# Kernel optimization log

Hardware: AMD Instinct MI355X
Metric: run time of the kernel (lower is better)

## Reference

```python
import jax, jax.numpy as jnp
import numpy as np

B, H, W, N, P = 8, 640, 640, 12, 256
MIN_PATCH_AREA = 4.0
SQRT2 = 1.41421356237
DEG20 = 20.0 * np.pi / 180.0
TOL = 0.2  # center jitter tolerance


def setup_inputs() -> dict:
    key = jax.random.key(0)
    k_img, k_patch, k_y, k_h, k_x, k_w = jax.random.split(key, 6)
    images = jax.random.uniform(k_img, (B, H, W, 3), minval=-1.0, maxval=1.0, dtype=jnp.float32)
    patch = jax.random.uniform(k_patch, (P, P, 3), minval=-1.0, maxval=1.0, dtype=jnp.float32)
    ymin = jax.random.uniform(k_y, (B, N), minval=0.0, maxval=H - 220.0)
    bh = jax.random.uniform(k_h, (B, N), minval=40.0, maxval=200.0)
    xmin = jax.random.uniform(k_x, (B, N), minval=0.0, maxval=W - 220.0)
    bw = jax.random.uniform(k_w, (B, N), minval=40.0, maxval=200.0)
    boxes = jnp.stack([ymin, xmin, ymin + bh, xmin + bw], axis=-1).astype(jnp.float32)
    scale = jnp.float32(0.4)
    return {"images": images, "boxes": boxes, "patch": patch, "scale": scale}


def _bilinear(img, py, px):
    # img: [P,P,3]; py/px: [H,W] continuous source coords; edge-clamped bilinear
    Pd = img.shape[0]
    y0 = jnp.floor(py); x0 = jnp.floor(px)
    wy = (py - y0)[..., None]; wx = (px - x0)[..., None]
    y0i = jnp.clip(y0.astype(jnp.int32), 0, Pd - 1)
    x0i = jnp.clip(x0.astype(jnp.int32), 0, Pd - 1)
    y1i = jnp.clip(y0i + 1, 0, Pd - 1)
    x1i = jnp.clip(x0i + 1, 0, Pd - 1)
    v00 = img[y0i, x0i]; v01 = img[y0i, x1i]
    v10 = img[y1i, x0i]; v11 = img[y1i, x1i]
    return (1 - wy) * ((1 - wx) * v00 + wx * v01) + wy * ((1 - wx) * v10 + wx * v11)


def _apply_box(image, patch_m, box, key, scale, yy, xx):
    kc1, kc2, ka, kd, kn = jax.random.split(key, 5)
    ymin, xmin, ymax, xmax = box[0], box[1], box[2], box[3]
    h = ymax - ymin; w = xmax - xmin
    longer = jnp.maximum(h, w)
    patch_size = jnp.floor(longer * scale)          # create(): floor(longer*scale)
    diag = jnp.minimum(SQRT2 * patch_size, float(W))
    jy = (jax.random.uniform(kc1, ()) - 0.5) * TOL * h
    jx = (jax.random.uniform(kc2, ()) - 0.5) * TOL * w
    oy = ymin + h / 2.0 + jy
    ox = xmin + w / 2.0 + jx
    ymin_p = jnp.maximum(oy - diag / 2.0, 0.0)
    xmin_p = jnp.maximum(ox - diag / 2.0, 0.0)
    ymin_p = jnp.where(ymin_p + diag > H, H - diag, ymin_p)
    xmin_p = jnp.where(xmin_p + diag > W, W - diag, xmin_p)
    valid_box = patch_size * patch_size > MIN_PATCH_AREA  # min-area filter
    # int32 casts in tf == floor on nonnegative values
    y0f = jnp.floor(ymin_p); x0f = jnp.floor(xmin_p)
    phf = patch_size; diagf = jnp.floor(diag)
    top = jnp.floor((diagf - phf) / 2.0)            # pad offset
    angle = (jax.random.uniform(ka, ()) * 2.0 - 1.0) * DEG20
    delta = (jax.random.uniform(kd, ()) * 2.0 - 1.0) * 0.3  # random_brightness
    # inverse warp: image pixel -> padded-rotated patch coords
    u = yy - y0f; v = xx - x0f
    inside = (u >= 0) & (u < diagf) & (v >= 0) & (v < diagf)
    c = (diagf - 1.0) / 2.0
    ca = jnp.cos(angle); sa = jnp.sin(angle)
    sv = ca * (v - c) - sa * (u - c) + c
    su = sa * (v - c) + ca * (u - c) + c
    ry = su - top; rx = sv - top                     # coords in resized ph x pw patch
    src_ok = (ry >= 0) & (ry <= phf - 1) & (rx >= 0) & (rx <= phf - 1)
    safe_ph = jnp.maximum(phf, 1.0)
    py = (ry + 0.5) * (P / safe_ph) - 0.5            # half-pixel-center resize map
    px = (rx + 0.5) * (P / safe_ph) - 0.5
    vals = _bilinear(patch_m, py, px)                # [H,W,3]
    noise = jax.random.uniform(kn, vals.shape, minval=-0.01, maxval=0.01)
    vals = jnp.clip(vals + noise + delta, -1.0, 1.0)
    mask = (inside & src_ok & valid_box)[..., None]
    return jnp.where(mask, vals, image)              # tensor_scatter_nd_update + bg fill


def _patch_one_image(image, boxes, patch, scale, key):
    kw, kb, ks = jax.random.split(key, 3)
    wmul = 0.5 + 0.1 * jax.random.normal(kw, (1, 1, 3))
    badd = 0.01 * jax.random.normal(kb, (1, 1, 3))
    p = jnp.clip(wmul * patch + badd, -1.0, 1.0)     # random_print_adjust
    p = jnp.clip(p + (jnp.mean(image) - jnp.mean(p)), -1.0, 1.0)  # brightness match
    yy, xx = jnp.meshgrid(jnp.arange(H, dtype=jnp.float32),
                          jnp.arange(W, dtype=jnp.float32), indexing="ij")
    box_keys = jax.random.split(ks, boxes.shape[0])

    def body(img, bk):
        box, k = bk
        return _apply_box(img, p, box, k, scale, yy, xx), None

    img, _ = jax.lax.scan(body, image, (boxes, box_keys))
    return img


def reference(images, boxes, patch, scale):
    key = jax.random.key(42)
    img_keys = jax.random.split(key, images.shape[0])
    return jax.vmap(lambda im, bx, k: _patch_one_image(im, bx, patch, scale, k))(images, boxes, img_keys)
```

## Files before the change

kernel.cpp:

```cpp
#include <hip/hip_runtime.h>
#include <stdint.h>


#define IMG_ELEMS   1228800
#define NPIX        409600
#define PATCH_ELEMS 196608
#define WB_OFF 2048
#define BP_OFF 2112

#define TF_R(r) { x0 += x1; x1 = (x1 << r) | (x1 >> (32 - r)); x1 ^= x0; }

__device__ __forceinline__ void tf2x32(uint32_t k0, uint32_t k1,
                                       uint32_t c0, uint32_t c1,
                                       uint32_t& o0, uint32_t& o1) {
  uint32_t k2 = k0 ^ k1 ^ 0x1BD11BDAu;
  uint32_t x0 = c0 + k0, x1 = c1 + k1;
  TF_R(13) TF_R(15) TF_R(26) TF_R(6)
  x0 += k1; x1 += k2 + 1u;
  TF_R(17) TF_R(29) TF_R(16) TF_R(24)
  x0 += k2; x1 += k0 + 2u;
  TF_R(13) TF_R(15) TF_R(26) TF_R(6)
  x0 += k0; x1 += k1 + 3u;
  TF_R(17) TF_R(29) TF_R(16) TF_R(24)
  x0 += k1; x1 += k2 + 4u;
  TF_R(13) TF_R(15) TF_R(26) TF_R(6)
  x0 += k2; x1 += k0 + 5u;
  o0 = x0; o1 = x1;
}

__device__ __forceinline__ void split_key(uint32_t k0, uint32_t k1, uint32_t j,
                                          uint32_t& o0, uint32_t& o1) {
  tf2x32(k0, k1, 0u, j, o0, o1);
}

__device__ __forceinline__ uint32_t rbits32(uint32_t k0, uint32_t k1, uint32_t i) {
  uint32_t o0, o1;
  tf2x32(k0, k1, 0u, i, o0, o1);
  return o0 ^ o1;
}

__device__ __forceinline__ float u01(uint32_t bits) {
  return __uint_as_float((bits >> 9) | 0x3f800000u) - 1.0f;
}

__device__ __forceinline__ float erfinv_f(float x) {
  #pragma clang fp contract(off)
  float w = -log1pf(-(x * x));
  float p;
  if (w < 5.0f) {
    w = w - 2.5f;
    p = 2.81022636e-08f;
    p = 3.43273939e-07f + p * w;
    p = -3.5233877e-06f + p * w;
    p = -4.39150654e-06f + p * w;
    p = 0.00021858087f + p * w;
    p = -0.00125372503f + p * w;
    p = -0.00417768164f + p * w;
    p = 0.246640727f + p * w;
    p = 1.50140941f + p * w;
  } else {
    w = sqrtf(w) - 3.0f;
    p = -0.000200214257f;
    p = 0.000100950558f + p * w;
    p = 0.00134934322f + p * w;
    p = -0.00367342844f + p * w;
    p = 0.00573950773f + p * w;
    p = -0.0076224613f + p * w;
    p = 0.00943887047f + p * w;
    p = 1.00167406f + p * w;
    p = 2.83297682f + p * w;
  }
  return p * x;
}

__device__ __forceinline__ void wb_compute(int b, float* wm, float* bd) {
  #pragma clang fp contract(off)
  uint32_t ik0, ik1; split_key(0u, 42u, (uint32_t)b, ik0, ik1);
  uint32_t kw0, kw1; split_key(ik0, ik1, 0u, kw0, kw1);
  uint32_t kb0, kb1; split_key(ik0, ik1, 1u, kb0, kb1);
  const float lo  = __uint_as_float(0xBF7FFFFFu);
  const float SQ2 = (float)1.4142135623730951;
  for (int c = 0; c < 3; ++c) {
    float f  = u01(rbits32(kw0, kw1, (uint32_t)c));
    float u  = fmaxf(lo, __fadd_rn(__fmul_rn(f, 2.0f), lo));
    wm[c] = __fadd_rn(0.5f, __fmul_rn(0.1f, __fmul_rn(SQ2, erfinv_f(u))));
    float f2 = u01(rbits32(kb0, kb1, (uint32_t)c));
    float u2 = fmaxf(lo, __fadd_rn(__fmul_rn(f2, 2.0f), lo));
    bd[c] = __fmul_rn(0.01f, __fmul_rn(SQ2, erfinv_f(u2)));
  }
}

__global__ __launch_bounds__(256) void k_sums(const float4* __restrict__ img,
                                              const float4* __restrict__ patch,
                                              const float* __restrict__ boxes,
                                              const float* __restrict__ scale_p,
                                              float* __restrict__ wsf) {
  #pragma clang fp contract(off)
  int b = blockIdx.y;
  int bx = blockIdx.x;
  double* Pd = (double*)wsf;
  int tid = threadIdx.x;

  if (bx == 120) {
    if (b != 0) return;
    float scale = scale_p[0];
    if (tid < 8) {
      float wm[3], bd[3];
      wb_compute(tid, wm, bd);
      #pragma unroll
      for (int c = 0; c < 3; ++c) {
        wsf[WB_OFF + tid * 8 + c] = wm[c];
        wsf[WB_OFF + tid * 8 + 4 + c] = bd[c];
      }
    }
    if (tid >= 32 && tid < 128) {
      int t = tid - 32;
      int ib = t / 12, n = t % 12;
      uint32_t ik0, ik1; split_key(0u, 42u, (uint32_t)ib, ik0, ik1);
      uint32_t ks0, ks1; split_key(ik0, ik1, 2u, ks0, ks1);
      uint32_t bk0, bk1; split_key(ks0, ks1, (uint32_t)n, bk0, bk1);
      uint32_t kc10, kc11; split_key(bk0, bk1, 0u, kc10, kc11);
      uint32_t kc20, kc21; split_key(bk0, bk1, 1u, kc20, kc21);
      uint32_t ka0,  ka1;  split_key(bk0, bk1, 2u, ka0,  ka1);
      uint32_t kd0,  kd1;  split_key(bk0, bk1, 3u, kd0,  kd1);
      uint32_t kn0,  kn1;  split_key(bk0, bk1, 4u, kn0,  kn1);

      const float* bxp = boxes + (ib * 12 + n) * 4;
      float ymin = bxp[0], xmin = bxp[1], ymax = bxp[2], xmax = bxp[3];
      float h  = __fsub_rn(ymax, ymin);
      float ww = __fsub_rn(xmax, xmin);
      float longer = fmaxf(h, ww);
      float patch_size = floorf(__fmul_rn(longer, scale));
      float diag = fminf(__fmul_rn((float)1.41421356237, patch_size), 640.0f);
      float u1 = u01(rbits32(kc10, kc11, 0u));
      float u2 = u01(rbits32(kc20, kc21, 0u));
      float jy = __fmul_rn(__fmul_rn(__fsub_rn(u1, 0.5f), 0.2f), h);
      float jx = __fmul_rn(__fmul_rn(__fsub_rn(u2, 0.5f), 0.2f), ww);
      float oy = __fadd_rn(__fadd_rn(ymin, __fmul_rn(h, 0.5f)), jy);
      float ox = __fadd_rn(__fadd_rn(xmin, __fmul_rn(ww, 0.5f)), jx);
      float ymin_p = fmaxf(__fsub_rn(oy, __fmul_rn(diag, 0.5f)), 0.0f);
      float xmin_p = fmaxf(__fsub_rn(ox, __fmul_rn(diag, 0.5f)), 0.0f);
      ymin_p = (__fadd_rn(ymin_p, diag) > 640.0f) ? __fsub_rn(640.0f, diag) : ymin_p;
      xmin_p = (__fadd_rn(xmin_p, diag) > 640.0f) ? __fsub_rn(640.0f, diag) : xmin_p;
      float valid = (__fmul_rn(patch_size, patch_size) > 4.0f) ? 1.0f : 0.0f;
      float y0f = floorf(ymin_p), x0f = floorf(xmin_p);
      float phf = patch_size, diagf = floorf(diag);
      float top = floorf(__fmul_rn(__fsub_rn(diagf, phf), 0.5f));
      float ua = u01(rbits32(ka0, ka1, 0u));
      float angle = __fmul_rn(__fsub_rn(__fmul_rn(ua, 2.0f), 1.0f),
                              (float)0.3490658503988659);
      float ud = u01(rbits32(kd0, kd1, 0u));
      float delta = __fmul_rn(__fsub_rn(__fmul_rn(ud, 2.0f), 1.0f), 0.3f);
      float cc = __fmul_rn(__fsub_rn(diagf, 1.0f), 0.5f);
      float ca = (float)cos((double)angle);
      float sa = (float)sin((double)angle);
      float safe_ph = fmaxf(phf, 1.0f);
      float q = __fdiv_rn(256.0f, safe_ph);

      float* Pp = wsf + BP_OFF + (ib * 12 + n) * 16;
      Pp[0] = y0f;  Pp[1] = x0f;  Pp[2] = diagf; Pp[3] = phf;
      Pp[4] = top;  Pp[5] = cc;   Pp[6] = ca;    Pp[7] = sa;
      Pp[8] = delta; Pp[9] = valid;
      Pp[10] = __uint_as_float(kn0); Pp[11] = __uint_as_float(kn1);
      Pp[12] = q;
    }
    return;
  }

  double s = 0.0;
  int slot;
  if (bx < 120) {
    slot = b * 120 + bx;
    const float4* p = img + (size_t)b * (IMG_ELEMS / 4);
    const uint32_t stride = 120u * 256u;
    for (uint32_t i = bx * 256u + tid; i < (uint32_t)(IMG_ELEMS / 4); i += stride) {
      float4 v = p[i];
      s += (double)v.x + (double)v.y + (double)v.z + (double)v.w;
    }
  } else {
    slot = 960 + b * 8 + (bx - 121);
    __shared__ float pwb[8];
    if (tid == 0) {
      float wm[3], bd[3];
      wb_compute(b, wm, bd);
      #pragma unroll
      for (int c = 0; c < 3; ++c) { pwb[c] = wm[c]; pwb[4 + c] = bd[c]; }
    }
    __syncthreads();
    float wm[3] = {pwb[0], pwb[1], pwb[2]};
    float bd[3] = {pwb[4], pwb[5], pwb[6]};
    const uint32_t stride = 8u * 256u;
    for (uint32_t i = (bx - 121u) * 256u + tid; i < (uint32_t)(PATCH_ELEMS / 4);
         i += stride) {
      float4 v = patch[i];
      uint32_t c = (4u * i) % 3u;
      float f[4] = {v.x, v.y, v.z, v.w};
      #pragma unroll
      for (int j = 0; j < 4; ++j) {
        float val = __fadd_rn(__fmul_rn(wm[c], f[j]), bd[c]);
        val = fminf(fmaxf(val, -1.0f), 1.0f);
        s += (double)val;
        c = (c == 2u) ? 0u : (c + 1u);
      }
    }
  }
  for (int off = 32; off > 0; off >>= 1) s += __shfl_down(s, off, 64);
  __shared__ double sd[4];
  if ((tid & 63) == 0) sd[tid >> 6] = s;
  __syncthreads();
  if (tid == 0) Pd[slot] = sd[0] + sd[1] + sd[2] + sd[3];
}

__global__ __launch_bounds__(256) void k_main(const float4* __restrict__ img4,
                                              const float* __restrict__ wsf,
                                              const float* __restrict__ patch,
                                              float4* __restrict__ out4) {
  #pragma clang fp contract(off)
  __shared__ float bp[192];
  __shared__ int cand[13];
  __shared__ float s_dm;
  __shared__ double s_tot[2];
  int b = blockIdx.y;
  int tid = threadIdx.x;
  const double* Pd = (const double*)wsf;
  const float* params = wsf + BP_OFF;
  if (tid < 192) bp[tid] = params[b * 192 + tid];
  if (tid >= 64 && tid < 128) {
    int i = tid - 64;
    double s = Pd[b * 120 + i] + ((i + 64 < 120) ? Pd[b * 120 + i + 64] : 0.0);
    for (int off = 32; off > 0; off >>= 1) s += __shfl_down(s, off, 64);
    if (i == 0) s_tot[0] = s;
  }
  if (tid >= 128 && tid < 192) {
    int j = tid - 128;
    double s = (j < 8) ? Pd[960 + b * 8 + j] : 0.0;
    for (int off = 32; off > 0; off >>= 1) s += __shfl_down(s, off, 64);
    if (j == 0) s_tot[1] = s;
  }
  __syncthreads();
  if (tid == 0) {
    int pix_first = blockIdx.x * 1024;
    int y_first = pix_first / 640;
    int y_last  = (pix_first + 1023) / 640;
    float yl = (float)y_first, yh = (float)y_last;
    int cnt = 0;
    for (int n = 11; n >= 0; --n) {
      const float* Pp = &bp[n * 16];
      if (Pp[9] == 0.0f) continue;
      float y0f = Pp[0], diagf = Pp[2];
      if (yh < y0f || yl >= __fadd_rn(y0f, diagf)) continue;
      cand[1 + cnt] = n; ++cnt;
    }
    cand[0] = cnt;
    float mi = (float)(s_tot[0] / (double)IMG_ELEMS);
    float mp = (float)(s_tot[1] / (double)PATCH_ELEMS);
    s_dm = __fsub_rn(mi, mp);
  }
  __syncthreads();
  int ncand = cand[0];

  int pix0 = blockIdx.x * 1024 + tid * 4;
  int y = pix0 / 640;
  int x0 = pix0 - y * 640;
  float yf = (float)y;

  size_t base4 = ((size_t)b * NPIX + (size_t)pix0) * 3u / 4u;
  float4 o0 = img4[base4], o1 = img4[base4 + 1], o2 = img4[base4 + 2];
  float ov[12] = {o0.x, o0.y, o0.z, o0.w, o1.x, o1.y, o1.z, o1.w,
                  o2.x, o2.y, o2.z, o2.w};

  if (ncand > 0) {
    float dm = s_dm;
    const float* wb = wsf + WB_OFF + b * 8;
    #pragma unroll
    for (int j = 0; j < 4; ++j) {
      float xf = (float)(x0 + j);
      int winner = -1;
      float ry = 0.0f, rx = 0.0f;
      for (int ci = 0; ci < ncand; ++ci) {
        int n = cand[1 + ci];
        const float* Pp = &bp[n * 16];
        float u = __fsub_rn(yf, Pp[0]);
        float v = __fsub_rn(xf, Pp[1]);
        float diagf = Pp[2];
        if (!(u >= 0.0f && u < diagf && v >= 0.0f && v < diagf)) continue;
        float cc = Pp[5], ca = Pp[6], sa = Pp[7];
        float vc = __fsub_rn(v, cc), uc = __fsub_rn(u, cc);
        float sv = __fadd_rn(__fsub_rn(__fmul_rn(ca, vc), __fmul_rn(sa, uc)), cc);
        float su = __fadd_rn(__fadd_rn(__fmul_rn(sa, vc), __fmul_rn(ca, uc)), cc);
        float top = Pp[4], phf = Pp[3];
        float ry_ = __fsub_rn(su, top);
        float rx_ = __fsub_rn(sv, top);
        float ph1 = __fsub_rn(phf, 1.0f);
        if (!(ry_ >= 0.0f && ry_ <= ph1 && rx_ >= 0.0f && rx_ <= ph1)) continue;
        winner = n; ry = ry_; rx = rx_;
        break;
      }
      if (winner >= 0) {
        const float* Pp = &bp[winner * 16];
        float q = Pp[12], delta = Pp[8];
        uint32_t kn0 = __float_as_uint(Pp[10]), kn1 = __float_as_uint(Pp[11]);
        float py = __fsub_rn(__fmul_rn(__fadd_rn(ry, 0.5f), q), 0.5f);
        float px = __fsub_rn(__fmul_rn(__fadd_rn(rx, 0.5f), q), 0.5f);
        float fy = floorf(py), fx = floorf(px);
        float wy = __fsub_rn(py, fy), wx = __fsub_rn(px, fx);
        int y0i = min(max((int)fy, 0), 255);
        int x0i = min(max((int)fx, 0), 255);
        int y1i = min(y0i + 1, 255);
        int x1i = min(x0i + 1, 255);
        int i00 = (y0i * 256 + x0i) * 3, i01 = (y0i * 256 + x1i) * 3;
        int i10 = (y1i * 256 + x0i) * 3, i11 = (y1i * 256 + x1i) * 3;
        float omwx = __fsub_rn(1.0f, wx), omwy = __fsub_rn(1.0f, wy);
        int pix = pix0 + j;
        #pragma unroll
        for (int ch = 0; ch < 3; ++ch) {
          float wmc = wb[ch], bdc = wb[4 + ch];
          float v00 = fminf(fmaxf(__fadd_rn(fminf(fmaxf(__fadd_rn(__fmul_rn(wmc, patch[i00 + ch]), bdc), -1.0f), 1.0f), dm), -1.0f), 1.0f);
          float v01 = fminf(fmaxf(__fadd_rn(fminf(fmaxf(__fadd_rn(__fmul_rn(wmc, patch[i01 + ch]), bdc), -1.0f), 1.0f), dm), -1.0f), 1.0f);
          float v10 = fminf(fmaxf(__fadd_rn(fminf(fmaxf(__fadd_rn(__fmul_rn(wmc, patch[i10 + ch]), bdc), -1.0f), 1.0f), dm), -1.0f), 1.0f);
          float v11 = fminf(fmaxf(__fadd_rn(fminf(fmaxf(__fadd_rn(__fmul_rn(wmc, patch[i11 + ch]), bdc), -1.0f), 1.0f), dm), -1.0f), 1.0f);
          float t_ = __fadd_rn(__fmul_rn(omwx, v00), __fmul_rn(wx, v01));
          float b_ = __fadd_rn(__fmul_rn(omwx, v10), __fmul_rn(wx, v11));
          float bil = __fadd_rn(__fmul_rn(omwy, t_), __fmul_rn(wy, b_));
          uint32_t ni = (uint32_t)pix * 3u + (uint32_t)ch;
          float nf = u01(rbits32(kn0, kn1, ni));
          float noise = fmaxf(-0.01f, __fadd_rn(__fmul_rn(nf, 0.02f), -0.01f));
          float val = __fadd_rn(__fadd_rn(bil, noise), delta);
          ov[j * 3 + ch] = fminf(fmaxf(val, -1.0f), 1.0f);
        }
      }
    }
  }
  out4[base4]     = make_float4(ov[0], ov[1], ov[2], ov[3]);
  out4[base4 + 1] = make_float4(ov[4], ov[5], ov[6], ov[7]);
  out4[base4 + 2] = make_float4(ov[8], ov[9], ov[10], ov[11]);
}

extern "C" void kernel_launch(void* const* d_in, const int* in_sizes, int n_in,
                              void* d_out, int out_size, void* d_ws, size_t ws_size,
                              hipStream_t stream) {
  const float* images = (const float*)d_in[0];
  const float* boxes  = (const float*)d_in[1];
  const float* patch  = (const float*)d_in[2];
  const float* scale  = (const float*)d_in[3];
  float* wsf = (float*)d_ws;

  hipLaunchKernelGGL(k_sums, dim3(129, 8), dim3(256), 0, stream,
                     (const float4*)images, (const float4*)patch, boxes, scale,
                     wsf);
  hipLaunchKernelGGL(k_main, dim3(400, 8), dim3(256), 0, stream,
                     (const float4*)images, wsf, patch, (float4*)d_out);
}
```

Baseline: 126.8 us.

## Fuse image copy into sum pass and scatter patches per box

The reduction kernel now writes the input image to the output while it reads it for the mean, so the image is read only once. The per-pixel main kernel is replaced by a per-box kernel with a grid over boxes and a 128x128 local window, which writes only the pixels a patch covers. Each pixel checks whether a later valid box covers it and skips if so, which keeps the last-box-wins order. The risks are uncoalesced scattered stores, a fixed 128-wide window that assumes the diagonal never exceeds 128, and the repeated overlap test per pixel.

```diff
diff --git a/kernel.cpp b/kernel.cpp
--- a/kernel.cpp
+++ b/kernel.cpp
@@ -91,6 +91,7 @@
 }
 
 __global__ __launch_bounds__(256) void k_sums(const float4* __restrict__ img,
+                                              float4* __restrict__ out4,
                                               const float4* __restrict__ patch,
                                               const float* __restrict__ boxes,
                                               const float* __restrict__ scale_p,
@@ -172,9 +173,11 @@
   if (bx < 120) {
     slot = b * 120 + bx;
     const float4* p = img + (size_t)b * (IMG_ELEMS / 4);
+    float4* o = out4 + (size_t)b * (IMG_ELEMS / 4);
     const uint32_t stride = 120u * 256u;
     for (uint32_t i = bx * 256u + tid; i < (uint32_t)(IMG_ELEMS / 4); i += stride) {
       float4 v = p[i];
+      o[i] = v;
       s += (double)v.x + (double)v.y + (double)v.z + (double)v.w;
     }
   } else {
@@ -211,16 +214,15 @@
   if (tid == 0) Pd[slot] = sd[0] + sd[1] + sd[2] + sd[3];
 }
 
-__global__ __launch_bounds__(256) void k_main(const float4* __restrict__ img4,
-                                              const float* __restrict__ wsf,
-                                              const float* __restrict__ patch,
-                                              float4* __restrict__ out4) {
+__global__ __launch_bounds__(256) void k_patch(const float* __restrict__ wsf,
+                                               const float* __restrict__ patch,
+                                               float* __restrict__ out) {
   #pragma clang fp contract(off)
   __shared__ float bp[192];
-  __shared__ int cand[13];
   __shared__ float s_dm;
   __shared__ double s_tot[2];
-  int b = blockIdx.y;
+  int b = blockIdx.z;
+  int n = blockIdx.y;
   int tid = threadIdx.x;
   const double* Pd = (const double*)wsf;
   const float* params = wsf + BP_OFF;
@@ -239,101 +241,98 @@
   }
   __syncthreads();
   if (tid == 0) {
-    int pix_first = blockIdx.x * 1024;
-    int y_first = pix_first / 640;
-    int y_last  = (pix_first + 1023) / 640;
-    float yl = (float)y_first, yh = (float)y_last;
-    int cnt = 0;
-    for (int n = 11; n >= 0; --n) {
-      const float* Pp = &bp[n * 16];
-      if (Pp[9] == 0.0f) continue;
-      float y0f = Pp[0], diagf = Pp[2];
-      if (yh < y0f || yl >= __fadd_rn(y0f, diagf)) continue;
-      cand[1 + cnt] = n; ++cnt;
-    }
-    cand[0] = cnt;
     float mi = (float)(s_tot[0] / (double)IMG_ELEMS);
     float mp = (float)(s_tot[1] / (double)PATCH_ELEMS);
     s_dm = __fsub_rn(mi, mp);
   }
   __syncthreads();
-  int ncand = cand[0];
-
-  int pix0 = blockIdx.x * 1024 + tid * 4;
-  int y = pix0 / 640;
-  int x0 = pix0 - y * 640;
+
+  const float* Pp = &bp[n * 16];
+  if (Pp[9] == 0.0f) return;
+  float diagf = Pp[2];
+  int idx = blockIdx.x * 1024 + tid * 4;
+  int u = idx >> 7;
+  int v0 = idx & 127;
+  float uf = (float)u;
+  if (uf >= diagf) return;
+
+  float y0f = Pp[0], x0f = Pp[1];
+  int y = (int)y0f + u;
   float yf = (float)y;
-
-  size_t base4 = ((size_t)b * NPIX + (size_t)pix0) * 3u / 4u;
-  float4 o0 = img4[base4], o1 = img4[base4 + 1], o2 = img4[base4 + 2];
-  float ov[12] = {o0.x, o0.y, o0.z, o0.w, o1.x, o1.y, o1.z, o1.w,
-                  o2.x, o2.y, o2.z, o2.w};
-
-  if (ncand > 0) {
-    float dm = s_dm;
-    const float* wb = wsf + WB_OFF + b * 8;
+  float cc = Pp[5], ca = Pp[6], sa = Pp[7];
+  float top = Pp[4], phf = Pp[3];
+  float ph1 = __fsub_rn(phf, 1.0f);
+  float q = Pp[12], delta = Pp[8];
+  uint32_t kn0 = __float_as_uint(Pp[10]), kn1 = __float_as_uint(Pp[11]);
+  float dm = s_dm;
+  const float* wb = wsf + WB_OFF + b * 8;
+  float uc = __fsub_rn(uf, cc);
+
+  #pragma unroll
+  for (int j = 0; j < 4; ++j) {
+    int vi = v0 + j;
+    float vf = (float)vi;
+    if (vf >= diagf) continue;
+    float vc = __fsub_rn(vf, cc);
+    float sv = __fadd_rn(__fsub_rn(__fmul_rn(ca, vc), __fmul_rn(sa, uc)), cc);
+    float su = __fadd_rn(__fadd_rn(__fmul_rn(sa, vc), __fmul_rn(ca, uc)), cc);
+    float ry = __fsub_rn(su, top);
+    float rx = __fsub_rn(sv, top);
+    if (!(ry >= 0.0f && ry <= ph1 && rx >= 0.0f && rx <= ph1)) continue;
+
+    int x = (int)x0f + vi;
+    float xf = (float)x;
+    bool taken = false;
+    for (int m = 11; m > n; --m) {
+      const float* Pm = &bp[m * 16];
+      if (Pm[9] == 0.0f) continue;
+      float um = __fsub_rn(yf, Pm[0]);
+      float vm = __fsub_rn(xf, Pm[1]);
+      float dgm = Pm[2];
+      if (!(um >= 0.0f && um < dgm && vm >= 0.0f && vm < dgm)) continue;
+      float ccm = Pm[5], cam = Pm[6], sam = Pm[7];
+      float vcm = __fsub_rn(vm, ccm), ucm = __fsub_rn(um, ccm);
+      float svm = __fadd_rn(__fsub_rn(__fmul_rn(cam, vcm), __fmul_rn(sam, ucm)), ccm);
+      float sum_ = __fadd_rn(__fadd_rn(__fmul_rn(sam, vcm), __fmul_rn(cam, ucm)), ccm);
+      float rym = __fsub_rn(sum_, Pm[4]);
+      float rxm = __fsub_rn(svm, Pm[4]);
+      float phm1 = __fsub_rn(Pm[3], 1.0f);
+      if (rym >= 0.0f && rym <= phm1 && rxm >= 0.0f && rxm <= phm1) {
+        taken = true; break;
+      }
+    }
+    if (taken) continue;
+
+    float py = __fsub_rn(__fmul_rn(__fadd_rn(ry, 0.5f), q), 0.5f);
+    float px = __fsub_rn(__fmul_rn(__fadd_rn(rx, 0.5f), q), 0.5f);
+    float fy = floorf(py), fx = floorf(px);
+    float wy = __fsub_rn(py, fy), wx = __fsub_rn(px, fx);
+    int y0i = min(max((int)fy, 0), 255);
+    int x0i = min(max((int)fx, 0), 255);
+    int y1i = min(y0i + 1, 255);
+    int x1i = min(x0i + 1, 255);
+    int i00 = (y0i * 256 + x0i) * 3, i01 = (y0i * 256 + x1i) * 3;
+    int i10 = (y1i * 256 + x0i) * 3, i11 = (y1i * 256 + x1i) * 3;
+    float omwx = __fsub_rn(1.0f, wx), omwy = __fsub_rn(1.0f, wy);
+    int pix = y * 640 + x;
+    size_t obase = ((size_t)b * NPIX + (size_t)pix) * 3u;
     #pragma unroll
-    for (int j = 0; j < 4; ++j) {
-      float xf = (float)(x0 + j);
-      int winner = -1;
-      float ry = 0.0f, rx = 0.0f;
-      for (int ci = 0; ci < ncand; ++ci) {
-        int n = cand[1 + ci];
-        const float* Pp = &bp[n * 16];
-        float u = __fsub_rn(yf, Pp[0]);
-        float v = __fsub_rn(xf, Pp[1]);
-        float diagf = Pp[2];
-        if (!(u >= 0.0f && u < diagf && v >= 0.0f && v < diagf)) continue;
-        float cc = Pp[5], ca = Pp[6], sa = Pp[7];
-        float vc = __fsub_rn(v, cc), uc = __fsub_rn(u, cc);
-        float sv = __fadd_rn(__fsub_rn(__fmul_rn(ca, vc), __fmul_rn(sa, uc)), cc);
-        float su = __fadd_rn(__fadd_rn(__fmul_rn(sa, vc), __fmul_rn(ca, uc)), cc);
-        float top = Pp[4], phf = Pp[3];
-        float ry_ = __fsub_rn(su, top);
-        float rx_ = __fsub_rn(sv, top);
-        float ph1 = __fsub_rn(phf, 1.0f);
-        if (!(ry_ >= 0.0f && ry_ <= ph1 && rx_ >= 0.0f && rx_ <= ph1)) continue;
-        winner = n; ry = ry_; rx = rx_;
-        break;
-      }
-      if (winner >= 0) {
-        const float* Pp = &bp[winner * 16];
-        float q = Pp[12], delta = Pp[8];
-        uint32_t kn0 = __float_as_uint(Pp[10]), kn1 = __float_as_uint(Pp[11]);
-        float py = __fsub_rn(__fmul_rn(__fadd_rn(ry, 0.5f), q), 0.5f);
-        float px = __fsub_rn(__fmul_rn(__fadd_rn(rx, 0.5f), q), 0.5f);
-        float fy = floorf(py), fx = floorf(px);
-        float wy = __fsub_rn(py, fy), wx = __fsub_rn(px, fx);
-        int y0i = min(max((int)fy, 0), 255);
-        int x0i = min(max((int)fx, 0), 255);
-        int y1i = min(y0i + 1, 255);
-        int x1i = min(x0i + 1, 255);
-        int i00 = (y0i * 256 + x0i) * 3, i01 = (y0i * 256 + x1i) * 3;
-        int i10 = (y1i * 256 + x0i) * 3, i11 = (y1i * 256 + x1i) * 3;
-        float omwx = __fsub_rn(1.0f, wx), omwy = __fsub_rn(1.0f, wy);
-        int pix = pix0 + j;
-        #pragma unroll
-        for (int ch = 0; ch < 3; ++ch) {
-          float wmc = wb[ch], bdc = wb[4 + ch];
-          float v00 = fminf(fmaxf(__fadd_rn(fminf(fmaxf(__fadd_rn(__fmul_rn(wmc, patch[i00 + ch]), bdc), -1.0f), 1.0f), dm), -1.0f), 1.0f);
-          float v01 = fminf(fmaxf(__fadd_rn(fminf(fmaxf(__fadd_rn(__fmul_rn(wmc, patch[i01 + ch]), bdc), -1.0f), 1.0f), dm), -1.0f), 1.0f);
-          float v10 = fminf(fmaxf(__fadd_rn(fminf(fmaxf(__fadd_rn(__fmul_rn(wmc, patch[i10 + ch]), bdc), -1.0f), 1.0f), dm), -1.0f), 1.0f);
-          float v11 = fminf(fmaxf(__fadd_rn(fminf(fmaxf(__fadd_rn(__fmul_rn(wmc, patch[i11 + ch]), bdc), -1.0f), 1.0f), dm), -1.0f), 1.0f);
-          float t_ = __fadd_rn(__fmul_rn(omwx, v00), __fmul_rn(wx, v01));
-          float b_ = __fadd_rn(__fmul_rn(omwx, v10), __fmul_rn(wx, v11));
-          float bil = __fadd_rn(__fmul_rn(omwy, t_), __fmul_rn(wy, b_));
-          uint32_t ni = (uint32_t)pix * 3u + (uint32_t)ch;
-          float nf = u01(rbits32(kn0, kn1, ni));
-          float noise = fmaxf(-0.01f, __fadd_rn(__fmul_rn(nf, 0.02f), -0.01f));
-          float val = __fadd_rn(__fadd_rn(bil, noise), delta);
-          ov[j * 3 + ch] = fminf(fmaxf(val, -1.0f), 1.0f);
-        }
-      }
-    }
-  }
-  out4[base4]     = make_float4(ov[0], ov[1], ov[2], ov[3]);
-  out4[base4 + 1] = make_float4(ov[4], ov[5], ov[6], ov[7]);
-  out4[base4 + 2] = make_float4(ov[8], ov[9], ov[10], ov[11]);
+    for (int ch = 0; ch < 3; ++ch) {
+      float wmc = wb[ch], bdc = wb[4 + ch];
+      float v00 = fminf(fmaxf(__fadd_rn(fminf(fmaxf(__fadd_rn(__fmul_rn(wmc, patch[i00 + ch]), bdc), -1.0f), 1.0f), dm), -1.0f), 1.0f);
+      float v01 = fminf(fmaxf(__fadd_rn(fminf(fmaxf(__fadd_rn(__fmul_rn(wmc, patch[i01 + ch]), bdc), -1.0f), 1.0f), dm), -1.0f), 1.0f);
+      float v10 = fminf(fmaxf(__fadd_rn(fminf(fmaxf(__fadd_rn(__fmul_rn(wmc, patch[i10 + ch]), bdc), -1.0f), 1.0f), dm), -1.0f), 1.0f);
+      float v11 = fminf(fmaxf(__fadd_rn(fminf(fmaxf(__fadd_rn(__fmul_rn(wmc, patch[i11 + ch]), bdc), -1.0f), 1.0f), dm), -1.0f), 1.0f);
+      float t_ = __fadd_rn(__fmul_rn(omwx, v00), __fmul_rn(wx, v01));
+      float b_ = __fadd_rn(__fmul_rn(omwx, v10), __fmul_rn(wx, v11));
+      float bil = __fadd_rn(__fmul_rn(omwy, t_), __fmul_rn(wy, b_));
+      uint32_t ni = (uint32_t)pix * 3u + (uint32_t)ch;
+      float nf = u01(rbits32(kn0, kn1, ni));
+      float noise = fmaxf(-0.01f, __fadd_rn(__fmul_rn(nf, 0.02f), -0.01f));
+      float val = __fadd_rn(__fadd_rn(bil, noise), delta);
+      out[obase + ch] = fminf(fmaxf(val, -1.0f), 1.0f);
+    }
+  }
 }
 
 extern "C" void kernel_launch(void* const* d_in, const int* in_sizes, int n_in,
@@ -346,8 +345,8 @@
   float* wsf = (float*)d_ws;
 
   hipLaunchKernelGGL(k_sums, dim3(129, 8), dim3(256), 0, stream,
-                     (const float4*)images, (const float4*)patch, boxes, scale,
-                     wsf);
-  hipLaunchKernelGGL(k_main, dim3(400, 8), dim3(256), 0, stream,
-                     (const float4*)images, wsf, patch, (float4*)d_out);
-}
+                     (const float4*)images, (float4*)d_out,
+                     (const float4*)patch, boxes, scale, wsf);
+  hipLaunchKernelGGL(k_patch, dim3(16, 12, 8), dim3(256), 0, stream,
+                     wsf, patch, (float*)d_out);
+}
```

New measurement: 126.4 us. About the same (-0.3%).
